# Optimization experiments

Measured on AMD Instinct MI355X. Metric: run time of the kernel, lower is better.

## Reference

```python
import jax, jax.numpy as jnp
import numpy as np

BS = 64          # batch size (bs = x.shape[0] / prev_num_nodes)
N_COARSE = 2562  # prev_num_nodes (refinement level r)
N_FINE = 10242   # num_nodes (refinement level r+1)
E_FINE = 61440   # directed edges per sample (~6 per mesh vertex)
C_IN, C_OUT = 128, 64


def setup_inputs() -> dict:
    key = jax.random.key(0)
    k1, k2, k3 = jax.random.split(key, 3)
    x = jax.random.normal(k1, (BS * N_COARSE, C_IN), jnp.float32)
    # xavier-uniform-like init per reset_parameters (scale immaterial for correctness)
    W = jax.random.normal(k2, (C_IN, C_OUT), jnp.float32) * (1.0 / np.sqrt(C_IN))
    b = jnp.zeros((C_OUT,), jnp.float32)  # bias init to 0 per reset_parameters
    # per-sample random fine-graph edges, block-shifted like check_bs does
    e = jax.random.randint(k3, (2, BS, E_FINE), 0, N_FINE)
    shifts = jnp.arange(BS, dtype=e.dtype) * N_FINE
    edge_index = (e + shifts[None, :, None]).reshape(2, BS * E_FINE)
    # coarse vertices are the first N_COARSE fine vertices of each block
    unpool_mask = (jnp.arange(N_COARSE, dtype=jnp.int64)[None, :]
                   + (jnp.arange(BS, dtype=jnp.int64) * N_FINE)[:, None]).reshape(-1)
    return {"x": x, "W": W, "b": b, "edge_index": edge_index,
            "unpool_mask": unpool_mask}


def reference(x, W, b, edge_index, unpool_mask):
    N = BS * N_FINE  # total fine nodes (static, = max(edge_index)+1 in original)
    # --- unpooler: scatter coarse features into fine node positions ---
    up = jnp.zeros((N, x.shape[1]), x.dtype).at[unpool_mask].set(x)
    # --- GCN convolution with self-loops and symmetric normalization ---
    h = up @ W  # [N, C_OUT]
    src, dst = edge_index[0], edge_index[1]
    ones = jnp.ones(src.shape, h.dtype)
    deg = jax.ops.segment_sum(ones, dst, num_segments=N) + 1.0  # +1 self-loop
    norm = jax.lax.rsqrt(deg)  # [N]
    coef = (norm[src] * norm[dst])[:, None]          # edge normalization
    agg = jax.ops.segment_sum(h[src] * coef, dst, num_segments=N)
    agg = agg + h * (norm * norm)[:, None]           # self-loop contribution
    # --- ELU activation ---
    return jax.nn.elu(agg + b)
```

## Files before the change

### kernel.cpp

```cpp
#include <hip/hip_runtime.h>
#include <hip/hip_bf16.h>
#include <math.h>

#define CIN 128
#define COUT 64
#define BM 128
#define KC 64
#define BSAMP 64
#define NFINE 10242
#define NCOARSE 2562
#define NRNG 4
#define RS 2561
#define HT 1024
#define NCLS 17
#define SEGCAP 20480
#define CPAD 16

typedef float f32x4 __attribute__((ext_vector_type(4)));

__global__ __launch_bounds__(256) void k_zero(int* __restrict__ cur, int n) {
    int i = blockIdx.x * 256 + threadIdx.x;
    if (i < n) cur[i] = 0;
}

__global__ __launch_bounds__(256) void k_prep(const int4* __restrict__ src4, const int4* __restrict__ dst4,
                                              unsigned* __restrict__ pk, int* __restrict__ cur,
                                              int EPS, int bps) {
    __shared__ unsigned bbuf[NRNG][1024];
    __shared__ int bcnt[NRNG];
    __shared__ int gb[NRNG];
    int t = threadIdx.x;
    int b  = blockIdx.x / bps;
    int il = (blockIdx.x % bps) * 256 + t;
    int n4 = EPS / 4;
    if (t < NRNG) bcnt[t] = 0;
    __syncthreads();
    if (il < n4) {
        size_t i = (size_t)b * n4 + il;
        int4 s = src4[i], d = dst4[i];
        int base = b * NFINE;
#define COMP(c) { \
        int ls = d.c - base; \
        if ((unsigned)ls < (unsigned)NFINE) { \
            int rri = ls / RS; \
            int sl = s.c - base; \
            unsigned rc = ((unsigned)sl < (unsigned)NCOARSE) ? (unsigned)(b * NCOARSE + sl + 1) : 0u; \
            unsigned pv = ((unsigned)(ls - rri * RS) << 18) | rc; \
            int p = atomicAdd(&bcnt[rri], 1); \
            bbuf[rri][p] = pv; } }
        COMP(x) COMP(y) COMP(z) COMP(w)
#undef COMP
    }
    __syncthreads();
    if (t < NRNG) gb[t] = atomicAdd(&cur[(b * NRNG + t) * CPAD], bcnt[t]);
    __syncthreads();
#pragma unroll
    for (int rr = 0; rr < NRNG; ++rr) {
        int n = bcnt[rr];
        int g0 = gb[rr];
        unsigned* seg = pk + (size_t)(b * NRNG + rr) * SEGCAP;
        for (int i = t; i < n; i += 256) {
            int pos = g0 + i;
            if (pos < SEGCAP) seg[pos] = bbuf[rr][i];
        }
    }
}

__global__ __launch_bounds__(HT) void k_build(const unsigned* __restrict__ pk, const int* __restrict__ cur,
                                              int2* __restrict__ meta, float* __restrict__ normc,
                                              int* __restrict__ vals, int* __restrict__ ord,
                                              int* __restrict__ gctr) {
    __shared__ int   lh[RS];
    __shared__ int   sm[HT];
    __shared__ int   ccnt[NCLS];
    __shared__ int   gbase;
    int t = threadIdx.x;
    int b = blockIdx.x / NRNG, r = blockIdx.x % NRNG;
    int lo = r * RS;
    int nlocal = min(RS, NFINE - lo);
    int rebase = b * NFINE + lo;
    for (int j = t; j < nlocal; j += HT) lh[j] = 0;
    if (t < NCLS) ccnt[t] = 0;
    __syncthreads();

    const unsigned* seg = pk + (size_t)(b * NRNG + r) * SEGCAP;
    int ne = min(cur[(b * NRNG + r) * CPAD], SEGCAP);
    for (int i = t; i < ne; i += HT) {
        unsigned u = seg[i];
        int l = (int)(u >> 18);
        int rc = (int)(u & 0x3FFFFu);
        if (l < nlocal) atomicAdd(&lh[l], 1 + (rc ? 65536 : 0));
    }
    __syncthreads();

    int mj[3], degk[3], selfk[3], cls[3], rank[3];
    int psum = 0;
#pragma unroll
    for (int k = 0; k < 3; ++k) {
        int idx = t + k * HT;
        int m = 0, dg = 0, sf = 0;
        if (idx < nlocal) {
            int c = lh[idx];
            int slocal = lo + idx;
            sf = (slocal < NCOARSE) ? (b * NCOARSE + slocal + 1) : 0;
            m = (c >> 16) + (sf ? 1 : 0);
            dg = (c & 0xFFFF) + 1;
            cls[k] = min(m, NCLS - 1);
            rank[k] = atomicAdd(&ccnt[cls[k]], 1);
        }
        mj[k] = m; degk[k] = dg; selfk[k] = sf;
        psum += m;
    }
    sm[t] = psum; __syncthreads();
    for (int off = 1; off < HT; off <<= 1) {
        int add = (t >= off) ? sm[t - off] : 0;
        __syncthreads();
        sm[t] += add;
        __syncthreads();
    }
    if (t == HT - 1) gbase = atomicAdd(gctr, sm[HT - 1]);
    if (t == 0) {
        int run = 0;
#pragma unroll
        for (int c = 0; c < NCLS; ++c) { int v = ccnt[c]; ccnt[c] = run; run += v; }
    }
    __syncthreads();

    int run = gbase + sm[t] - psum;
#pragma unroll
    for (int k = 0; k < 3; ++k) {
        int idx = t + k * HT;
        if (idx < nlocal) {
            int gf = rebase + idx;
            meta[gf] = make_int2(run, mj[k] | (degk[k] << 16));
            ord[rebase + ccnt[cls[k]] + rank[k]] = gf;
            int cur2 = run;
            if (selfk[k]) {
                int rv = selfk[k] - 1;
                normc[rv] = rsqrtf((float)degk[k]);
                vals[cur2] = rv;
                ++cur2;
            }
            lh[idx] = cur2;
            run += mj[k];
        }
    }
    __syncthreads();

    for (int i = t; i < ne; i += HT) {
        unsigned u = seg[i];
        int l = (int)(u >> 18);
        int rc = (int)(u & 0x3FFFFu);
        if (rc && l < nlocal) {
            int pos = atomicAdd(&lh[l], 1);
            vals[pos] = rc - 1;
        }
    }
}

__global__ __launch_bounds__(256) void k_gemm(const float* __restrict__ x, const float* __restrict__ W,
                                              const float* __restrict__ normc,
                                              __hip_bfloat16* __restrict__ h, int M) {
    __shared__ float sXT[KC][BM];
    __shared__ float sW[KC][COUT];
    int t = threadIdx.x;
    int row0 = blockIdx.x * BM;
    int tr = (t & 31) * 4;
    int tc = (t >> 5) * 8;
    float acc[4][8];
#pragma unroll
    for (int i = 0; i < 4; ++i)
#pragma unroll
        for (int j = 0; j < 8; ++j) acc[i][j] = 0.f;

    for (int k0 = 0; k0 < CIN; k0 += KC) {
        __syncthreads();
#pragma unroll
        for (int it = 0; it < 8; ++it) {
            int i = it * 256 + t;
            int row = i >> 4;
            int kq  = (i & 15) * 4;
            int gr = row0 + row;
            float4 v = (gr < M) ? *reinterpret_cast<const float4*>(&x[(size_t)gr * CIN + k0 + kq])
                                : make_float4(0.f, 0.f, 0.f, 0.f);
            sXT[kq + 0][row] = v.x;
            sXT[kq + 1][row] = v.y;
            sXT[kq + 2][row] = v.z;
            sXT[kq + 3][row] = v.w;
        }
#pragma unroll
        for (int it = 0; it < 4; ++it) {
            int i = it * 256 + t;
            int kk = i >> 4;
            int cq = (i & 15) * 4;
            *reinterpret_cast<float4*>(&sW[kk][cq]) =
                *reinterpret_cast<const float4*>(&W[(size_t)(k0 + kk) * COUT + cq]);
        }
        __syncthreads();
#pragma unroll 8
        for (int k = 0; k < KC; ++k) {
            float4 xa = *reinterpret_cast<const float4*>(&sXT[k][tr]);
            float4 wa = *reinterpret_cast<const float4*>(&sW[k][tc]);
            float4 wb = *reinterpret_cast<const float4*>(&sW[k][tc + 4]);
            float xs[4] = { xa.x, xa.y, xa.z, xa.w };
            float ws[8] = { wa.x, wa.y, wa.z, wa.w, wb.x, wb.y, wb.z, wb.w };
#pragma unroll
            for (int i = 0; i < 4; ++i)
#pragma unroll
                for (int j = 0; j < 8; ++j)
                    acc[i][j] = fmaf(xs[i], ws[j], acc[i][j]);
        }
    }
#pragma unroll
    for (int i = 0; i < 4; ++i) {
        int gr = row0 + tr + i;
        if (gr < M) {
            float sc = normc[gr];
            alignas(16) __hip_bfloat16 tmp[8];
#pragma unroll
            for (int j = 0; j < 8; ++j) tmp[j] = __float2bfloat16(acc[i][j] * sc);
            *reinterpret_cast<float4*>(&h[(size_t)gr * COUT + tc]) = *reinterpret_cast<const float4*>(tmp);
        }
    }
}

__global__ __launch_bounds__(256) void k_gather(const __hip_bfloat16* __restrict__ h, const int2* __restrict__ meta,
                                                const int* __restrict__ vals, const int* __restrict__ ord,
                                                const float* __restrict__ b, float* __restrict__ out, int N16) {
    int wid  = (blockIdx.x * 256 + threadIdx.x) >> 6;
    int lane = threadIdx.x & 63;
    if (wid >= N16) return;
    int g  = lane >> 4;
    int il = lane & 15;
    int base = wid * 16;
    f32x4 bb = *reinterpret_cast<const f32x4*>(&b[il * 4]);

    int nid[4], bg[4], mm[4], mx[4];
    float nf[4];
    f32x4 acc[4];
    int mmax = 0;
#pragma unroll
    for (int s = 0; s < 4; ++s) {
        nid[s] = ord[base + 4 * s + g];
        int2 Mi = meta[nid[s]];
        bg[s] = Mi.x;
        mm[s] = Mi.y & 0xFFFF;
        nf[s] = rsqrtf((float)(Mi.y >> 16));
        int m1 = max(mm[s], __shfl_xor(mm[s], 16));
        mx[s] = max(m1, __shfl_xor(m1, 32));
        acc[s] = (f32x4)(0.f);
        mmax = max(mmax, mx[s]);
    }
    const char* hb = (const char*)h;
    for (int j = 0; j < mmax; ++j) {
#pragma unroll
        for (int s = 0; s < 4; ++s) {
            if (j < mx[s]) {
                bool act = j < mm[s];
                int e = act ? vals[bg[s] + j] : 0;
                uint2 hw = act ? *(const uint2*)(hb + (((size_t)(unsigned)e) << 7) + il * 8)
                               : make_uint2(0u, 0u);
                acc[s].x += __uint_as_float(hw.x << 16);
                acc[s].y += __uint_as_float(hw.x & 0xFFFF0000u);
                acc[s].z += __uint_as_float(hw.y << 16);
                acc[s].w += __uint_as_float(hw.y & 0xFFFF0000u);
            }
        }
    }
#pragma unroll
    for (int s = 0; s < 4; ++s) {
        f32x4 v;
        v.x = fmaf(acc[s].x, nf[s], bb.x);
        v.y = fmaf(acc[s].y, nf[s], bb.y);
        v.z = fmaf(acc[s].z, nf[s], bb.z);
        v.w = fmaf(acc[s].w, nf[s], bb.w);
        v.x = v.x > 0.f ? v.x : (__expf(v.x) - 1.0f);
        v.y = v.y > 0.f ? v.y : (__expf(v.y) - 1.0f);
        v.z = v.z > 0.f ? v.z : (__expf(v.z) - 1.0f);
        v.w = v.w > 0.f ? v.w : (__expf(v.w) - 1.0f);
        f32x4* dstp = (f32x4*)(out + ((size_t)(unsigned)nid[s]) * COUT + il * 4);
        __builtin_nontemporal_store(v, dstp);
    }
}

extern "C" void kernel_launch(void* const* d_in, const int* in_sizes, int n_in,
                              void* d_out, int out_size, void* d_ws, size_t ws_size,
                              hipStream_t stream) {
    const float* x    = (const float*)d_in[0];
    const float* W    = (const float*)d_in[1];
    const float* b    = (const float*)d_in[2];
    const int*   edge = (const int*)d_in[3];
    const int Mx = in_sizes[0] / CIN;
    const int E  = in_sizes[3] / 2;
    const int N  = out_size / COUT;
    const int EPS = E / BSAMP;

    const int* src = edge;
    const int* dst = edge + E;

    char* ws = (char*)d_ws;
    int2*  meta   = (int2*)ws;     ws += (size_t)N * 8;
    int*   cur    = (int*)ws;      ws += (256 * CPAD + 256) * 4;
    float* normc  = (float*)ws;    ws += (size_t)Mx * 4;
    int*   ord    = (int*)ws;      ws += (size_t)N * 4;
    __hip_bfloat16* h = (__hip_bfloat16*)ws;
    unsigned* pk  = (unsigned*)ws;
    {
        size_t hbytes  = (size_t)Mx * COUT * 2;
        size_t pkbytes = (size_t)BSAMP * NRNG * SEGCAP * 4;
        ws += (hbytes > pkbytes ? hbytes : pkbytes);
    }
    int*   vals   = (int*)ws;

    int* gctr = cur + 256 * CPAD;
    const int bps = (EPS / 4 + 255) / 256;
    const int nzero = 256 * CPAD + 1;

    k_zero  <<<(nzero + 255) / 256, 256, 0, stream>>>(cur, nzero);
    k_prep  <<<BSAMP * bps, 256, 0, stream>>>((const int4*)src, (const int4*)dst, pk, cur, EPS, bps);
    k_build <<<BSAMP * NRNG, HT, 0, stream>>>(pk, cur, meta, normc, vals, ord, gctr);
    k_gemm  <<<(Mx + BM - 1) / BM, 256, 0, stream>>>(x, W, normc, h, Mx);
    k_gather<<<((N / 16) * 64 + 255) / 256, 256, 0, stream>>>(h, meta, vals, ord, b, (float*)d_out, N / 16);
}
```

Measured before the change: 154.1 us.

## Use bf16 MFMA for GEMM and give each gather wave 32 nodes

The FP32 shared-memory SIMT GEMM is replaced by a bf16 MFMA 16x16x32 kernel. Each wave computes 16 rows, with W transposed into LDS and x converted to bf16 in registers. The gather kernel now handles 32 nodes per wave instead of 16, which raises memory-level parallelism per wave. Costs: x and W are rounded to bf16 before the multiply, h is stored with scattered 2-byte writes, and there is no bounds check on rows when M is not a multiple of 16.

```diff
diff --git a/kernel.cpp b/kernel.cpp
--- a/kernel.cpp
+++ b/kernel.cpp
@@ -4,8 +4,6 @@
 
 #define CIN 128
 #define COUT 64
-#define BM 128
-#define KC 64
 #define BSAMP 64
 #define NFINE 10242
 #define NCOARSE 2562
@@ -17,6 +15,7 @@
 #define CPAD 16
 
 typedef float f32x4 __attribute__((ext_vector_type(4)));
+typedef short s16x8 __attribute__((ext_vector_type(8)));
 
 __global__ __launch_bounds__(256) void k_zero(int* __restrict__ cur, int n) {
     int i = blockIdx.x * 256 + threadIdx.x;
@@ -161,86 +160,80 @@
 __global__ __launch_bounds__(256) void k_gemm(const float* __restrict__ x, const float* __restrict__ W,
                                               const float* __restrict__ normc,
                                               __hip_bfloat16* __restrict__ h, int M) {
-    __shared__ float sXT[KC][BM];
-    __shared__ float sW[KC][COUT];
+    __shared__ unsigned short sWT[COUT][CIN + 8];
     int t = threadIdx.x;
-    int row0 = blockIdx.x * BM;
-    int tr = (t & 31) * 4;
-    int tc = (t >> 5) * 8;
-    float acc[4][8];
-#pragma unroll
-    for (int i = 0; i < 4; ++i)
-#pragma unroll
-        for (int j = 0; j < 8; ++j) acc[i][j] = 0.f;
-
-    for (int k0 = 0; k0 < CIN; k0 += KC) {
-        __syncthreads();
-#pragma unroll
-        for (int it = 0; it < 8; ++it) {
-            int i = it * 256 + t;
-            int row = i >> 4;
-            int kq  = (i & 15) * 4;
-            int gr = row0 + row;
-            float4 v = (gr < M) ? *reinterpret_cast<const float4*>(&x[(size_t)gr * CIN + k0 + kq])
-                                : make_float4(0.f, 0.f, 0.f, 0.f);
-            sXT[kq + 0][row] = v.x;
-            sXT[kq + 1][row] = v.y;
-            sXT[kq + 2][row] = v.z;
-            sXT[kq + 3][row] = v.w;
-        }
-#pragma unroll
-        for (int it = 0; it < 4; ++it) {
-            int i = it * 256 + t;
-            int kk = i >> 4;
-            int cq = (i & 15) * 4;
-            *reinterpret_cast<float4*>(&sW[kk][cq]) =
-                *reinterpret_cast<const float4*>(&W[(size_t)(k0 + kk) * COUT + cq]);
-        }
-        __syncthreads();
-#pragma unroll 8
-        for (int k = 0; k < KC; ++k) {
-            float4 xa = *reinterpret_cast<const float4*>(&sXT[k][tr]);
-            float4 wa = *reinterpret_cast<const float4*>(&sW[k][tc]);
-            float4 wb = *reinterpret_cast<const float4*>(&sW[k][tc + 4]);
-            float xs[4] = { xa.x, xa.y, xa.z, xa.w };
-            float ws[8] = { wa.x, wa.y, wa.z, wa.w, wb.x, wb.y, wb.z, wb.w };
-#pragma unroll
-            for (int i = 0; i < 4; ++i)
-#pragma unroll
-                for (int j = 0; j < 8; ++j)
-                    acc[i][j] = fmaf(xs[i], ws[j], acc[i][j]);
-        }
-    }
-#pragma unroll
-    for (int i = 0; i < 4; ++i) {
-        int gr = row0 + tr + i;
-        if (gr < M) {
-            float sc = normc[gr];
-            alignas(16) __hip_bfloat16 tmp[8];
-#pragma unroll
-            for (int j = 0; j < 8; ++j) tmp[j] = __float2bfloat16(acc[i][j] * sc);
-            *reinterpret_cast<float4*>(&h[(size_t)gr * COUT + tc]) = *reinterpret_cast<const float4*>(tmp);
+    for (int i = t; i < CIN * COUT; i += 256) {
+        int k = i >> 6, c = i & 63;
+        __hip_bfloat16 v = __float2bfloat16(W[i]);
+        sWT[c][k] = *reinterpret_cast<unsigned short*>(&v);
+    }
+    __syncthreads();
+
+    int wid  = t >> 6;
+    int lane = t & 63;
+    int r0 = blockIdx.x * 64 + wid * 16;
+    if (r0 >= M) return;
+    int row = lane & 15;
+    int kg  = lane >> 4;
+
+    s16x8 bf[4][4];
+#pragma unroll
+    for (int ct = 0; ct < 4; ++ct)
+#pragma unroll
+        for (int ks = 0; ks < 4; ++ks)
+            bf[ct][ks] = *reinterpret_cast<const s16x8*>(&sWT[ct * 16 + row][ks * 32 + kg * 8]);
+
+    const float* xr = x + (size_t)(r0 + row) * CIN + kg * 8;
+    s16x8 af[4];
+#pragma unroll
+    for (int ks = 0; ks < 4; ++ks) {
+        float4 a0 = *reinterpret_cast<const float4*>(xr + ks * 32);
+        float4 a1 = *reinterpret_cast<const float4*>(xr + ks * 32 + 4);
+        alignas(16) __hip_bfloat16 tmp[8];
+        tmp[0] = __float2bfloat16(a0.x); tmp[1] = __float2bfloat16(a0.y);
+        tmp[2] = __float2bfloat16(a0.z); tmp[3] = __float2bfloat16(a0.w);
+        tmp[4] = __float2bfloat16(a1.x); tmp[5] = __float2bfloat16(a1.y);
+        tmp[6] = __float2bfloat16(a1.z); tmp[7] = __float2bfloat16(a1.w);
+        af[ks] = *reinterpret_cast<const s16x8*>(tmp);
+    }
+
+    f32x4 acc[4] = { (f32x4)(0.f), (f32x4)(0.f), (f32x4)(0.f), (f32x4)(0.f) };
+#pragma unroll
+    for (int ks = 0; ks < 4; ++ks)
+#pragma unroll
+        for (int ct = 0; ct < 4; ++ct)
+            acc[ct] = __builtin_amdgcn_mfma_f32_16x16x32_bf16(af[ks], bf[ct][ks], acc[ct], 0, 0, 0);
+
+    float sc[4];
+#pragma unroll
+    for (int j = 0; j < 4; ++j) sc[j] = normc[r0 + kg * 4 + j];
+#pragma unroll
+    for (int ct = 0; ct < 4; ++ct) {
+#pragma unroll
+        for (int j = 0; j < 4; ++j) {
+            int rr = r0 + kg * 4 + j;
+            h[(size_t)rr * COUT + ct * 16 + row] = __float2bfloat16(acc[ct][j] * sc[j]);
         }
     }
 }
 
 __global__ __launch_bounds__(256) void k_gather(const __hip_bfloat16* __restrict__ h, const int2* __restrict__ meta,
                                                 const int* __restrict__ vals, const int* __restrict__ ord,
-                                                const float* __restrict__ b, float* __restrict__ out, int N16) {
+                                                const float* __restrict__ b, float* __restrict__ out, int N32) {
     int wid  = (blockIdx.x * 256 + threadIdx.x) >> 6;
     int lane = threadIdx.x & 63;
-    if (wid >= N16) return;
+    if (wid >= N32) return;
     int g  = lane >> 4;
     int il = lane & 15;
-    int base = wid * 16;
+    int base = wid * 32;
     f32x4 bb = *reinterpret_cast<const f32x4*>(&b[il * 4]);
 
-    int nid[4], bg[4], mm[4], mx[4];
-    float nf[4];
-    f32x4 acc[4];
+    int nid[8], bg[8], mm[8], mx[8];
+    float nf[8];
+    f32x4 acc[8];
     int mmax = 0;
 #pragma unroll
-    for (int s = 0; s < 4; ++s) {
+    for (int s = 0; s < 8; ++s) {
         nid[s] = ord[base + 4 * s + g];
         int2 Mi = meta[nid[s]];
         bg[s] = Mi.x;
@@ -254,7 +247,7 @@
     const char* hb = (const char*)h;
     for (int j = 0; j < mmax; ++j) {
 #pragma unroll
-        for (int s = 0; s < 4; ++s) {
+        for (int s = 0; s < 8; ++s) {
             if (j < mx[s]) {
                 bool act = j < mm[s];
                 int e = act ? vals[bg[s] + j] : 0;
@@ -268,7 +261,7 @@
         }
     }
 #pragma unroll
-    for (int s = 0; s < 4; ++s) {
+    for (int s = 0; s < 8; ++s) {
         f32x4 v;
         v.x = fmaf(acc[s].x, nf[s], bb.x);
         v.y = fmaf(acc[s].y, nf[s], bb.y);
@@ -319,6 +312,6 @@
     k_zero  <<<(nzero + 255) / 256, 256, 0, stream>>>(cur, nzero);
     k_prep  <<<BSAMP * bps, 256, 0, stream>>>((const int4*)src, (const int4*)dst, pk, cur, EPS, bps);
     k_build <<<BSAMP * NRNG, HT, 0, stream>>>(pk, cur, meta, normc, vals, ord, gctr);
-    k_gemm  <<<(Mx + BM - 1) / BM, 256, 0, stream>>>(x, W, normc, h, Mx);
-    k_gather<<<((N / 16) * 64 + 255) / 256, 256, 0, stream>>>(h, meta, vals, ord, b, (float*)d_out, N / 16);
-}
+    k_gemm  <<<(Mx + 63) / 64, 256, 0, stream>>>(x, W, normc, h, Mx);
+    k_gather<<<((N / 32) * 64 + 255) / 256, 256, 0, stream>>>(h, meta, vals, ord, b, (float*)d_out, N / 32);
+}
```

New measurement: 149.8 us. 2.8% less time.
